# Optimization experiments

Measured on AMD Instinct MI355X. Metric: run time of the kernel, lower is better.

Reference implementation:

```python
import jax, jax.numpy as jnp
import numpy as np

B, N, C, K = 32, 4096, 768, 8

def setup_inputs() -> dict:
    key = jax.random.key(0)
    ks = jax.random.split(key, 5)
    x = jax.random.normal(ks[0], (B, N, C), dtype=jnp.float32)
    ln_gamma = jnp.ones((C,), dtype=jnp.float32)
    ln_beta = jnp.zeros((C,), dtype=jnp.float32)
    W1 = jax.random.normal(ks[1], (C, C), dtype=jnp.float32) / np.sqrt(C)
    b1 = jnp.zeros((C,), dtype=jnp.float32)
    W2 = jax.random.normal(ks[2], (C, K), dtype=jnp.float32) / np.sqrt(C)
    b2 = jnp.zeros((K,), dtype=jnp.float32)
    return {"x": x, "ln_gamma": ln_gamma, "ln_beta": ln_beta,
            "W1": W1, "b1": b1, "W2": W2, "b2": b2}

def reference(x, ln_gamma, ln_beta, W1, b1, W2, b2):
    # LayerNorm over last dim (eps matches torch default 1e-5)
    mu = jnp.mean(x, axis=-1, keepdims=True)
    var = jnp.mean(jnp.square(x - mu), axis=-1, keepdims=True)
    h = (x - mu) * jax.lax.rsqrt(var + 1e-5) * ln_gamma + ln_beta
    # Linear -> exact GELU -> Linear
    h = jax.nn.gelu(h @ W1 + b1, approximate=False)
    logits = h @ W2 + b2  # [B, N, K]
    # softmax over tokens (dim=1)
    attn = jax.nn.softmax(logits, axis=1)
    # weighted token pooling: [B,N,K],[B,N,C] -> [B,K,C]
    return jnp.einsum('bnk,bnc->bkc', attn, x)
```

## Files before the change

### kernel.cpp

```cpp
#include <hip/hip_runtime.h>
#include <hip/hip_fp16.h>

#define M_TOKENS (32*4096)
#define C_DIM 768
#define K_OUT 8

typedef _Float16 f16x8 __attribute__((ext_vector_type(8)));
typedef float f32x4 __attribute__((ext_vector_type(4)));

__device__ __forceinline__ void gl2lds16(const void* g, void* l) {
    __builtin_amdgcn_global_load_lds((const __attribute__((address_space(1))) void*)g,
                                     (__attribute__((address_space(3))) void*)l, 16, 0, 0);
}

__device__ __forceinline__ float gelu_exact(float x) {
    return 0.5f * x * (1.0f + erff(x * 0.70710678118654752440f));
}

__global__ __launch_bounds__(256) void prep_w1(const float* __restrict__ w1,
                                               const float* __restrict__ gamma,
                                               _Float16* __restrict__ w1t) {
    __shared__ float t[64][65];
    const int k0 = blockIdx.x * 64, n0 = blockIdx.y * 64;
    const int c = threadIdx.x & 63, r4 = threadIdx.x >> 6;
#pragma unroll
    for (int p = 0; p < 16; ++p) {
        const int r = p*4 + r4;
        t[r][c] = w1[(size_t)(k0 + r)*C_DIM + n0 + c];
    }
    __syncthreads();
    const float g = gamma[k0 + c];
#pragma unroll
    for (int p = 0; p < 16; ++p) {
        const int n = p*4 + r4;
        w1t[(size_t)(n0 + n)*C_DIM + k0 + c] = (_Float16)(t[c][n] * g);
    }
}

__global__ __launch_bounds__(256) void prep_b1(const float* __restrict__ w1,
                                               const float* __restrict__ beta,
                                               const float* __restrict__ b1,
                                               float* __restrict__ b1p) {
    const int n = blockIdx.x*256 + threadIdx.x;
    float s = b1[n];
    for (int k = 0; k < C_DIM; ++k) s += beta[k] * w1[(size_t)k*C_DIM + n];
    b1p[n] = s;
}

__global__ __launch_bounds__(256) void stats_kernel(const float* __restrict__ x,
                                                    float2* __restrict__ stats) {
    const int row = blockIdx.x*4 + (threadIdx.x >> 6);
    const int lane = threadIdx.x & 63;
    const float4* xr = (const float4*)(x + (size_t)row * C_DIM);
    float s = 0.f, s2 = 0.f;
#pragma unroll
    for (int i = 0; i < 3; ++i) {
        const float4 v = xr[lane + i*64];
        s  += v.x + v.y + v.z + v.w;
        s2 += v.x*v.x + v.y*v.y + v.z*v.z + v.w*v.w;
    }
#pragma unroll
    for (int m = 1; m < 64; m <<= 1) { s += __shfl_xor(s, m); s2 += __shfl_xor(s2, m); }
    if (lane == 0) {
        const float mu = s * (1.f/768.f);
        const float rs = rsqrtf(s2 * (1.f/768.f) - mu*mu + 1e-5f);
        stats[row] = make_float2(rs, -mu*rs);
    }
}

__global__ __launch_bounds__(256) void gemm1_kernel(const float* __restrict__ x,
        const float2* __restrict__ stats, const _Float16* __restrict__ w1t,
        const float* __restrict__ b1p, const float* __restrict__ w2,
        float* __restrict__ logits) {
    __shared__ __align__(16) union {
        struct { float a[128*64]; _Float16 b[128*64]; } s;
        _Float16 ht[128*136];
    } u;
    __shared__ float w2s[128*K_OUT];
    __shared__ float b1s[128];

    const int tid = threadIdx.x;
    const int wid = tid >> 6, lane = tid & 63;
    const int l15 = lane & 15, q = lane >> 4;
    const int wm = wid >> 1, wn = wid & 1;
    const int n0 = blockIdx.x * 128;
    const int m0 = blockIdx.y * 128;

    for (int i = tid; i < 128*K_OUT; i += 256) w2s[i] = w2[(size_t)n0*K_OUT + i];
    if (tid < 128) b1s[tid] = b1p[n0 + tid];

    float rsL[4], nmL[4];
#pragma unroll
    for (int mt = 0; mt < 4; ++mt) {
        const float2 st = stats[m0 + wm*64 + mt*16 + l15];
        rsL[mt] = st.x; nmL[mt] = st.y;
    }

    f32x4 acc[4][4] = {};

    for (int kt = 0; kt < 12; ++kt) {
        const int k0 = kt * 64;
#pragma unroll
        for (int i = 0; i < 8; ++i) {
            const int L = i*256 + tid;
            const int row = L >> 4, g = (L & 15) ^ (row & 15);
            gl2lds16(x + (size_t)(m0 + row)*C_DIM + k0 + g*4,
                     &u.s.a[(i*256 + wid*64)*4]);
        }
#pragma unroll
        for (int i = 0; i < 4; ++i) {
            const int L = i*256 + tid;
            const int row = L >> 3, j = (L & 7) ^ (row & 7);
            gl2lds16(w1t + (size_t)(n0 + row)*C_DIM + k0 + j*8,
                     &u.s.b[(i*256 + wid*64)*8]);
        }
        __syncthreads();
#pragma unroll
        for (int kk = 0; kk < 2; ++kk) {
            f16x8 af[4], bfr[4];
#pragma unroll
            for (int nt = 0; nt < 4; ++nt) {
                const int row = wn*64 + nt*16 + l15;
                const int j = (kk*4 + q) ^ (row & 7);
                af[nt] = *(const f16x8*)&u.s.b[row*64 + j*8];
            }
#pragma unroll
            for (int mt = 0; mt < 4; ++mt) {
                const int row = wm*64 + mt*16 + l15;
                const int gc = kk*8 + q*2;
                const int c0 = gc ^ (row & 15), c1 = (gc + 1) ^ (row & 15);
                const f32x4 v0 = *(const f32x4*)&u.s.a[row*64 + c0*4];
                const f32x4 v1 = *(const f32x4*)&u.s.a[row*64 + c1*4];
                f16x8 t;
#pragma unroll
                for (int j = 0; j < 4; ++j) {
                    t[j]   = (_Float16)(v0[j]*rsL[mt] + nmL[mt]);
                    t[4+j] = (_Float16)(v1[j]*rsL[mt] + nmL[mt]);
                }
                bfr[mt] = t;
            }
#pragma unroll
            for (int nt = 0; nt < 4; ++nt)
#pragma unroll
                for (int mt = 0; mt < 4; ++mt)
                    acc[nt][mt] = __builtin_amdgcn_mfma_f32_16x16x32_f16(
                        af[nt], bfr[mt], acc[nt][mt], 0, 0, 0);
        }
        __syncthreads();
    }

#pragma unroll
    for (int nt = 0; nt < 4; ++nt) {
#pragma unroll
        for (int mt = 0; mt < 4; ++mt) {
            const int token = wm*64 + mt*16 + l15;
            const int nl = wn*64 + nt*16 + q*4;
            union { _Float16 h[4]; uint2 uu; } pk;
#pragma unroll
            for (int r = 0; r < 4; ++r)
                pk.h[r] = (_Float16)gelu_exact(acc[nt][mt][r] + b1s[nl + r]);
            *(uint2*)&u.ht[token*136 + nl] = pk.uu;
        }
    }
    __syncthreads();

    f16x8 wf[4];
#pragma unroll
    for (int ks = 0; ks < 4; ++ks) {
        f16x8 t;
#pragma unroll
        for (int j = 0; j < 8; ++j) {
            const int kd = ks*32 + q*8 + j;
            t[j] = (_Float16)((l15 < K_OUT) ? w2s[kd*K_OUT + l15] : 0.f);
        }
        wf[ks] = t;
    }
#pragma unroll
    for (int t2 = 0; t2 < 2; ++t2) {
        const int tt = wid*2 + t2;
        f32x4 p = {};
#pragma unroll
        for (int ks = 0; ks < 4; ++ks) {
            const f16x8 a = *(const f16x8*)&u.ht[(tt*16 + l15)*136 + ks*32 + q*8];
            p = __builtin_amdgcn_mfma_f32_16x16x32_f16(a, wf[ks], p, 0, 0, 0);
        }
        if (l15 < K_OUT) {
#pragma unroll
            for (int r = 0; r < 4; ++r)
                atomicAdd(&logits[(size_t)(m0 + tt*16 + q*4 + r)*K_OUT + l15], p[r]);
        }
    }
}

__global__ __launch_bounds__(256) void softmax_kernel(float* p) {
    const int b = blockIdx.x >> 3, k = blockIdx.x & 7;
    const size_t base = ((size_t)b*4096)*K_OUT + k;
    const int tid = threadIdx.x;
    float r[16];
    float mx = -1e30f;
#pragma unroll
    for (int i = 0; i < 16; ++i) {
        r[i] = p[base + (size_t)(tid + i*256)*K_OUT];
        mx = fmaxf(mx, r[i]);
    }
#pragma unroll
    for (int m = 1; m < 64; m <<= 1) mx = fmaxf(mx, __shfl_xor(mx, m));
    __shared__ float redm[4], reds[4];
    if ((tid & 63) == 0) redm[tid >> 6] = mx;
    __syncthreads();
    mx = fmaxf(fmaxf(redm[0], redm[1]), fmaxf(redm[2], redm[3]));
    float s = 0.f;
#pragma unroll
    for (int i = 0; i < 16; ++i) { r[i] = __expf(r[i] - mx); s += r[i]; }
#pragma unroll
    for (int m = 1; m < 64; m <<= 1) s += __shfl_xor(s, m);
    if ((tid & 63) == 0) reds[tid >> 6] = s;
    __syncthreads();
    s = reds[0] + reds[1] + reds[2] + reds[3];
    const float inv = 1.f / s;
#pragma unroll
    for (int i = 0; i < 16; ++i)
        p[base + (size_t)(tid + i*256)*K_OUT] = r[i] * inv;
}

__global__ __launch_bounds__(192) void pool_kernel(const float* __restrict__ x,
        const float* __restrict__ attn, float* __restrict__ out) {
    const int b = blockIdx.x, nc = blockIdx.y;
    const int t0 = nc * 128;
    __shared__ float as_[128*K_OUT];
    for (int i = threadIdx.x; i < 128*K_OUT; i += 192)
        as_[i] = attn[((size_t)b*4096 + t0)*K_OUT + i];
    __syncthreads();
    const int c = threadIdx.x * 4;
    float acc[K_OUT][4] = {};
    const float* xb = x + ((size_t)b*4096 + t0)*C_DIM + c;
    for (int i = 0; i < 128; ++i) {
        const float4 xv = *(const float4*)(xb + (size_t)i*C_DIM);
#pragma unroll
        for (int k = 0; k < K_OUT; ++k) {
            const float a = as_[i*K_OUT + k];
            acc[k][0] += a*xv.x; acc[k][1] += a*xv.y;
            acc[k][2] += a*xv.z; acc[k][3] += a*xv.w;
        }
    }
#pragma unroll
    for (int k = 0; k < K_OUT; ++k)
#pragma unroll
        for (int j = 0; j < 4; ++j)
            atomicAdd(&out[((size_t)b*K_OUT + k)*C_DIM + c + j], acc[k][j]);
}

extern "C" void kernel_launch(void* const* d_in, const int* in_sizes, int n_in,
                              void* d_out, int out_size, void* d_ws, size_t ws_size,
                              hipStream_t stream) {
    const float* x     = (const float*)d_in[0];
    const float* gamma = (const float*)d_in[1];
    const float* beta  = (const float*)d_in[2];
    const float* W1    = (const float*)d_in[3];
    const float* b1    = (const float*)d_in[4];
    const float* W2    = (const float*)d_in[5];
    (void)in_sizes; (void)n_in; (void)ws_size;

    float* out = (float*)d_out;

    char* ws = (char*)d_ws;
    float2*   stats  = (float2*)ws;
    _Float16* w1t    = (_Float16*)(ws + 1048576);
    float*    b1p    = (float*)(ws + 2228224);
    float*    logits = (float*)(ws + 2232320);

    (void)hipMemsetAsync(logits, 0, (size_t)M_TOKENS * K_OUT * 4, stream);
    (void)hipMemsetAsync(d_out, 0, (size_t)out_size * sizeof(float), stream);

    prep_w1<<<dim3(12, 12), 256, 0, stream>>>(W1, gamma, w1t);
    prep_b1<<<3, 256, 0, stream>>>(W1, beta, b1, b1p);
    stats_kernel<<<M_TOKENS/4, 256, 0, stream>>>(x, stats);
    gemm1_kernel<<<dim3(6, 1024), 256, 0, stream>>>(x, stats, w1t, b1p, W2, logits);
    softmax_kernel<<<256, 256, 0, stream>>>(logits);
    pool_kernel<<<dim3(32, 32), 192, 0, stream>>>(x, logits, out);
}
```

Before: 1.176 ms.

## Pre-normalize x to fp16 buffer and run fp16-only GEMM1 path

Adds an xnorm kernel that applies LayerNorm and writes x as fp16 into workspace. A new GEMM1 kernel then loads fp16 A tiles directly into LDS via global_load_lds, rather than loading fp32 x and normalizing inside the GEMM. This is meant to halve the GEMM's A-operand traffic, which is re-read by 6 column blocks, and to remove per-tile conversion work. The cost is an extra 200MB write plus read pass and a large workspace requirement, with the old path kept as a fallback. prep_b1 is also split across four thread groups per column with an LDS reduction.

```diff
diff --git a/kernel.cpp b/kernel.cpp
--- a/kernel.cpp
+++ b/kernel.cpp
@@ -41,11 +41,157 @@
                                                const float* __restrict__ beta,
                                                const float* __restrict__ b1,
                                                float* __restrict__ b1p) {
-    const int n = blockIdx.x*256 + threadIdx.x;
-    float s = b1[n];
-    for (int k = 0; k < C_DIM; ++k) s += beta[k] * w1[(size_t)k*C_DIM + n];
-    b1p[n] = s;
-}
+    __shared__ float red[256];
+    const int nl = threadIdx.x & 63;
+    const int n = blockIdx.x*64 + nl;
+    const int part = threadIdx.x >> 6;
+    float s = 0.f;
+    for (int k = part*192; k < part*192 + 192; ++k)
+        s += beta[k] * w1[(size_t)k*C_DIM + n];
+    red[threadIdx.x] = s;
+    __syncthreads();
+    if (part == 0)
+        b1p[n] = b1[n] + red[nl] + red[nl+64] + red[nl+128] + red[nl+192];
+}
+
+
+__global__ __launch_bounds__(256) void xnorm_kernel(const float* __restrict__ x,
+                                                    _Float16* __restrict__ xn) {
+    const int row = blockIdx.x*4 + (threadIdx.x >> 6);
+    const int lane = threadIdx.x & 63;
+    const float4* xr = (const float4*)(x + (size_t)row * C_DIM);
+    float4 v[3];
+    float s = 0.f, s2 = 0.f;
+#pragma unroll
+    for (int i = 0; i < 3; ++i) {
+        v[i] = xr[lane + i*64];
+        s  += v[i].x + v[i].y + v[i].z + v[i].w;
+        s2 += v[i].x*v[i].x + v[i].y*v[i].y + v[i].z*v[i].z + v[i].w*v[i].w;
+    }
+#pragma unroll
+    for (int m = 1; m < 64; m <<= 1) { s += __shfl_xor(s, m); s2 += __shfl_xor(s2, m); }
+    const float mu = s * (1.f/768.f);
+    const float rs = rsqrtf(s2 * (1.f/768.f) - mu*mu + 1e-5f);
+    const float nm = -mu * rs;
+    _Float16* xo = xn + (size_t)row * C_DIM;
+#pragma unroll
+    for (int i = 0; i < 3; ++i) {
+        union { _Float16 h[4]; uint2 uu; } pk;
+        pk.h[0] = (_Float16)(v[i].x*rs + nm);
+        pk.h[1] = (_Float16)(v[i].y*rs + nm);
+        pk.h[2] = (_Float16)(v[i].z*rs + nm);
+        pk.h[3] = (_Float16)(v[i].w*rs + nm);
+        *(uint2*)(xo + (size_t)(lane + i*64)*4) = pk.uu;
+    }
+}
+
+__global__ __launch_bounds__(256) void gemm1_h_kernel(const _Float16* __restrict__ xn,
+        const _Float16* __restrict__ w1t, const float* __restrict__ b1p,
+        const float* __restrict__ w2, float* __restrict__ logits) {
+    __shared__ __align__(16) union {
+        struct { _Float16 a[128*64]; _Float16 b[128*64]; } s;
+        _Float16 ht[128*136];
+    } u;
+    __shared__ float w2s[128*K_OUT];
+    __shared__ float b1s[128];
+
+    const int tid = threadIdx.x;
+    const int wid = tid >> 6, lane = tid & 63;
+    const int l15 = lane & 15, q = lane >> 4;
+    const int wm = wid >> 1, wn = wid & 1;
+    const int n0 = blockIdx.x * 128;
+    const int m0 = blockIdx.y * 128;
+
+    for (int i = tid; i < 128*K_OUT; i += 256) w2s[i] = w2[(size_t)n0*K_OUT + i];
+    if (tid < 128) b1s[tid] = b1p[n0 + tid];
+
+    f32x4 acc[4][4] = {};
+
+    for (int kt = 0; kt < 12; ++kt) {
+        const int k0 = kt * 64;
+#pragma unroll
+        for (int i = 0; i < 4; ++i) {
+            const int L = i*256 + tid;
+            const int row = L >> 3, j = (L & 7) ^ (row & 7);
+            gl2lds16(xn + (size_t)(m0 + row)*C_DIM + k0 + j*8,
+                     &u.s.a[(i*256 + wid*64)*8]);
+        }
+#pragma unroll
+        for (int i = 0; i < 4; ++i) {
+            const int L = i*256 + tid;
+            const int row = L >> 3, j = (L & 7) ^ (row & 7);
+            gl2lds16(w1t + (size_t)(n0 + row)*C_DIM + k0 + j*8,
+                     &u.s.b[(i*256 + wid*64)*8]);
+        }
+        __syncthreads();
+#pragma unroll
+        for (int kk = 0; kk < 2; ++kk) {
+            f16x8 af[4], bfr[4];
+#pragma unroll
+            for (int nt = 0; nt < 4; ++nt) {
+                const int row = wn*64 + nt*16 + l15;
+                const int j = (kk*4 + q) ^ (row & 7);
+                af[nt] = *(const f16x8*)&u.s.b[row*64 + j*8];
+            }
+#pragma unroll
+            for (int mt = 0; mt < 4; ++mt) {
+                const int row = wm*64 + mt*16 + l15;
+                const int j = (kk*4 + q) ^ (row & 7);
+                bfr[mt] = *(const f16x8*)&u.s.a[row*64 + j*8];
+            }
+#pragma unroll
+            for (int nt = 0; nt < 4; ++nt)
+#pragma unroll
+                for (int mt = 0; mt < 4; ++mt)
+                    acc[nt][mt] = __builtin_amdgcn_mfma_f32_16x16x32_f16(
+                        af[nt], bfr[mt], acc[nt][mt], 0, 0, 0);
+        }
+        __syncthreads();
+    }
+
+#pragma unroll
+    for (int nt = 0; nt < 4; ++nt) {
+#pragma unroll
+        for (int mt = 0; mt < 4; ++mt) {
+            const int token = wm*64 + mt*16 + l15;
+            const int nl = wn*64 + nt*16 + q*4;
+            union { _Float16 h[4]; uint2 uu; } pk;
+#pragma unroll
+            for (int r = 0; r < 4; ++r)
+                pk.h[r] = (_Float16)gelu_exact(acc[nt][mt][r] + b1s[nl + r]);
+            *(uint2*)&u.ht[token*136 + nl] = pk.uu;
+        }
+    }
+    __syncthreads();
+
+    f16x8 wf[4];
+#pragma unroll
+    for (int ks = 0; ks < 4; ++ks) {
+        f16x8 t;
+#pragma unroll
+        for (int j = 0; j < 8; ++j) {
+            const int kd = ks*32 + q*8 + j;
+            t[j] = (_Float16)((l15 < K_OUT) ? w2s[kd*K_OUT + l15] : 0.f);
+        }
+        wf[ks] = t;
+    }
+#pragma unroll
+    for (int t2 = 0; t2 < 2; ++t2) {
+        const int tt = wid*2 + t2;
+        f32x4 p = {};
+#pragma unroll
+        for (int ks = 0; ks < 4; ++ks) {
+            const f16x8 a = *(const f16x8*)&u.ht[(tt*16 + l15)*136 + ks*32 + q*8];
+            p = __builtin_amdgcn_mfma_f32_16x16x32_f16(a, wf[ks], p, 0, 0, 0);
+        }
+        if (l15 < K_OUT) {
+#pragma unroll
+            for (int r = 0; r < 4; ++r)
+                atomicAdd(&logits[(size_t)(m0 + tt*16 + q*4 + r)*K_OUT + l15], p[r]);
+        }
+    }
+}
+
 
 __global__ __launch_bounds__(256) void stats_kernel(const float* __restrict__ x,
                                                     float2* __restrict__ stats) {
@@ -68,7 +214,7 @@
     }
 }
 
-__global__ __launch_bounds__(256) void gemm1_kernel(const float* __restrict__ x,
+__global__ __launch_bounds__(256) void gemm1_ln_kernel(const float* __restrict__ x,
         const float2* __restrict__ stats, const _Float16* __restrict__ w1t,
         const float* __restrict__ b1p, const float* __restrict__ w2,
         float* __restrict__ logits) {
@@ -259,23 +405,43 @@
     const float* W1    = (const float*)d_in[3];
     const float* b1    = (const float*)d_in[4];
     const float* W2    = (const float*)d_in[5];
-    (void)in_sizes; (void)n_in; (void)ws_size;
+    (void)in_sizes; (void)n_in;
 
     float* out = (float*)d_out;
-
     char* ws = (char*)d_ws;
-    float2*   stats  = (float2*)ws;
-    _Float16* w1t    = (_Float16*)(ws + 1048576);
-    float*    b1p    = (float*)(ws + 2228224);
-    float*    logits = (float*)(ws + 2232320);
-
-    (void)hipMemsetAsync(logits, 0, (size_t)M_TOKENS * K_OUT * 4, stream);
-    (void)hipMemsetAsync(d_out, 0, (size_t)out_size * sizeof(float), stream);
-
-    prep_w1<<<dim3(12, 12), 256, 0, stream>>>(W1, gamma, w1t);
-    prep_b1<<<3, 256, 0, stream>>>(W1, beta, b1, b1p);
-    stats_kernel<<<M_TOKENS/4, 256, 0, stream>>>(x, stats);
-    gemm1_kernel<<<dim3(6, 1024), 256, 0, stream>>>(x, stats, w1t, b1p, W2, logits);
-    softmax_kernel<<<256, 256, 0, stream>>>(logits);
-    pool_kernel<<<dim3(32, 32), 192, 0, stream>>>(x, logits, out);
-}
+
+    const size_t XN_BYTES  = (size_t)M_TOKENS * C_DIM * 2;
+    const size_t NEED_NEW  = XN_BYTES + 1179648 + 4096 + 4194304;
+
+    if (ws_size >= NEED_NEW) {
+        _Float16* xn     = (_Float16*)ws;
+        _Float16* w1t    = (_Float16*)(ws + XN_BYTES);
+        float*    b1p    = (float*)(ws + XN_BYTES + 1179648);
+        float*    logits = (float*)(ws + XN_BYTES + 1179648 + 4096);
+
+        (void)hipMemsetAsync(logits, 0, (size_t)M_TOKENS * K_OUT * 4, stream);
+        (void)hipMemsetAsync(d_out, 0, (size_t)out_size * sizeof(float), stream);
+
+        prep_w1<<<dim3(12, 12), 256, 0, stream>>>(W1, gamma, w1t);
+        prep_b1<<<12, 256, 0, stream>>>(W1, beta, b1, b1p);
+        xnorm_kernel<<<M_TOKENS/4, 256, 0, stream>>>(x, xn);
+        gemm1_h_kernel<<<dim3(6, 1024), 256, 0, stream>>>(xn, w1t, b1p, W2, logits);
+        softmax_kernel<<<256, 256, 0, stream>>>(logits);
+        pool_kernel<<<dim3(32, 32), 192, 0, stream>>>(x, logits, out);
+    } else {
+        float2*   stats  = (float2*)ws;
+        _Float16* w1t    = (_Float16*)(ws + 1048576);
+        float*    b1p    = (float*)(ws + 2228224);
+        float*    logits = (float*)(ws + 2232320);
+
+        (void)hipMemsetAsync(logits, 0, (size_t)M_TOKENS * K_OUT * 4, stream);
+        (void)hipMemsetAsync(d_out, 0, (size_t)out_size * sizeof(float), stream);
+
+        prep_w1<<<dim3(12, 12), 256, 0, stream>>>(W1, gamma, w1t);
+        prep_b1<<<12, 256, 0, stream>>>(W1, beta, b1, b1p);
+        stats_kernel<<<M_TOKENS/4, 256, 0, stream>>>(x, stats);
+        gemm1_ln_kernel<<<dim3(6, 1024), 256, 0, stream>>>(x, stats, w1t, b1p, W2, logits);
+        softmax_kernel<<<256, 256, 0, stream>>>(logits);
+        pool_kernel<<<dim3(32, 32), 192, 0, stream>>>(x, logits, out);
+    }
+}
```

Result: faster. 1.079 ms (-8.2%).
